# Kernel optimization log

Hardware: AMD Instinct MI355X
Metric: run time of the kernel (lower is better)

Reference implementation:

```python
import jax, jax.numpy as jnp
import numpy as np

B, S, D, H = 4, 1024, 512, 8
NEG = -1e9


def setup_inputs() -> dict:
    key = jax.random.key(0)
    ks = jax.random.split(key, 16)
    s = 0.02
    inp = {
        "query": jax.random.normal(ks[0], (B, S, D), dtype=jnp.float32),
        "key": jax.random.normal(ks[1], (B, S, D), dtype=jnp.float32),
        "value": jax.random.normal(ks[2], (B, S, D), dtype=jnp.float32),
        "mask": jax.random.randint(ks[3], (B, 1, S), 0, 2, dtype=jnp.int32),
        "mask_p": jax.random.randint(ks[4], (B, 1, S), 0, 2, dtype=jnp.int32),
        # multi-head projections: d_model -> d_model*h
        "Wq": jax.random.normal(ks[5], (D, H * D), dtype=jnp.float32) * s,
        "bq": jnp.zeros((H * D,), dtype=jnp.float32),
        "Wk": jax.random.normal(ks[6], (D, H * D), dtype=jnp.float32) * s,
        "bk": jnp.zeros((H * D,), dtype=jnp.float32),
        "Wv": jax.random.normal(ks[7], (D, H * D), dtype=jnp.float32) * s,
        "bv": jnp.zeros((H * D,), dtype=jnp.float32),
        # single-head p-branch projections: d_model -> d_model
        "Wpq": jax.random.normal(ks[8], (D, D), dtype=jnp.float32) * s,
        "bpq": jnp.zeros((D,), dtype=jnp.float32),
        "Wpk": jax.random.normal(ks[9], (D, D), dtype=jnp.float32) * s,
        "bpk": jnp.zeros((D,), dtype=jnp.float32),
        "Wpv": jax.random.normal(ks[10], (D, D), dtype=jnp.float32) * s,
        "bpv": jnp.zeros((D,), dtype=jnp.float32),
        # output projection
        "Wo": jax.random.normal(ks[11], (D, D), dtype=jnp.float32) * s,
        "bo": jnp.zeros((D,), dtype=jnp.float32),
    }
    return inp


def _attn(q, k, v, mask4):
    # q,k,v: [B,h,S,d]; mask4: [B,1,1,S] or None. Dropout omitted (eval mode).
    d = q.shape[-1]
    scores = jnp.einsum('bhqd,bhkd->bhqk', q, k) / jnp.sqrt(jnp.asarray(d, q.dtype))
    if mask4 is not None:
        scores = jnp.where(mask4 == 0, jnp.asarray(NEG, scores.dtype), scores)
    p = jax.nn.softmax(scores, axis=-1)
    return jnp.einsum('bhqk,bhkd->bhqd', p, v)


def reference(query, key, value, mask, mask_p,
              Wq, bq, Wk, bk, Wv, bv,
              Wpq, bpq, Wpk, bpk, Wpv, bpv, Wo, bo):
    nb, sl, d = query.shape
    def proj(x, W, b, heads):
        return (x @ W + b).reshape(nb, sl, heads, d).transpose(0, 2, 1, 3)

    m4 = mask[:, None, :, :]    # [B,1,1,S]
    mp4 = mask_p[:, None, :, :]

    qx = proj(query, Wq, bq, H)
    kx = proj(key, Wk, bk, H)
    vx = proj(value, Wv, bv, H)
    x = _attn(qx, kx, vx, m4)            # [B,H,S,D]

    qp = proj(query, Wpq, bpq, 1)
    kp = proj(key, Wpk, bpk, 1)
    vp = proj(value, Wpv, bpv, 1)
    x_p = _attn(qp, kp, vp, mp4)         # [B,1,S,D]

    # squared distance per head, softmax over heads at each (b, s)
    dis = jnp.sum((x - x_p) ** 2, axis=3)          # [B,H,S]
    w = jax.nn.softmax(1.0 / (dis + 1e-9), axis=1)  # [B,H,S]
    output = jnp.einsum('bhs,bhsd->bsd', w, x)      # [B,S,D]

    mixed = output * 0.8 + x_p[:, 0] * 0.2
    return mixed @ Wo + bo
```

## Files before the change

### kernel.cpp

```cpp
#include <hip/hip_runtime.h>
#include <cstdint>

#define S_LEN   1024
#define D_DIM   512
#define H_HEADS 8
#define B_BATCH 4
#define NEGV    -1000000000.0f

typedef __bf16 bf16;
typedef __bf16 bf16x8 __attribute__((ext_vector_type(8)));
typedef __bf16 bf16x4 __attribute__((ext_vector_type(4)));
typedef float  f32x4  __attribute__((ext_vector_type(4)));

#define GLL16(gp, lp) __builtin_amdgcn_global_load_lds( \
    (const __attribute__((address_space(1))) void*)(gp), \
    (__attribute__((address_space(3))) void*)(lp), 16, 0, 0)

template<int MODE>
__global__ __launch_bounds__(256) void gemm_bt(
    const bf16* __restrict__ A, const bf16* __restrict__ B,
    void* __restrict__ Cout, const float* __restrict__ bias,
    const float* __restrict__ bias2, const int* __restrict__ mask,
    int N, int K, long zsA, long zsB, long zsC, float scale, int Hh)
{
  const int z = blockIdx.z;
  A += (long)z * zsA;
  B += (long)z * zsB;

  const int bm0 = blockIdx.x * 128;
  const int bn0 = blockIdx.y * 128;

  __shared__ __attribute__((aligned(16))) bf16 As[128 * 32];
  __shared__ __attribute__((aligned(16))) bf16 Bs[128 * 32];

  const int tid  = threadIdx.x;
  const int wid  = tid >> 6;
  const int lane = tid & 63;
  const int wm = (wid >> 1) * 64;
  const int wn = (wid & 1) * 64;

  const int srow = tid >> 2;
  const int scol = (tid & 3) * 8;
  const bf16* gA0 = A + (long)(bm0 + srow) * K + scol;
  const bf16* gA1 = A + (long)(bm0 + 64 + srow) * K + scol;
  const bf16* gB0 = B + (long)(bn0 + srow) * K + scol;
  const bf16* gB1 = B + (long)(bn0 + 64 + srow) * K + scol;
  bf16* lA0 = As + tid * 8;
  bf16* lA1 = As + 2048 + tid * 8;
  bf16* lB0 = Bs + tid * 8;
  bf16* lB1 = Bs + 2048 + tid * 8;

  const int lrow = lane & 15;
  const int lk   = (lane >> 4) * 8;
  const bf16* fA = As + (wm + lrow) * 32 + lk;
  const bf16* fB = Bs + (wn + lrow) * 32 + lk;

  f32x4 acc[4][4] = {};

  for (int k0 = 0; k0 < K; k0 += 32) {
    GLL16(gA0 + k0, lA0);
    GLL16(gA1 + k0, lA1);
    GLL16(gB0 + k0, lB0);
    GLL16(gB1 + k0, lB1);
    __syncthreads();
    bf16x8 af[4], bfr[4];
#pragma unroll
    for (int i = 0; i < 4; ++i) af[i]  = *(const bf16x8*)(fA + i * 16 * 32);
#pragma unroll
    for (int i = 0; i < 4; ++i) bfr[i] = *(const bf16x8*)(fB + i * 16 * 32);
#pragma unroll
    for (int mi = 0; mi < 4; ++mi)
#pragma unroll
      for (int ni = 0; ni < 4; ++ni)
        acc[mi][ni] = __builtin_amdgcn_mfma_f32_16x16x32_bf16(
            af[mi], bfr[ni], acc[mi][ni], 0, 0, 0);
    __syncthreads();
  }

  const int r0 = (lane >> 4) << 2;
  const int cn = lane & 15;

#pragma unroll
  for (int mi = 0; mi < 4; ++mi) {
#pragma unroll
    for (int ni = 0; ni < 4; ++ni) {
      const int n = bn0 + wn + ni * 16 + cn;
      float bv = 0.f;
      if constexpr (MODE != 4) {
        const float* bp = (z == 1 && bias2) ? bias2 : bias;
        if (bp) bv = bp[n];
      }
      int mk = 1;
      if constexpr (MODE == 4) mk = mask[(z / Hh) * S_LEN + n];
#pragma unroll
      for (int r = 0; r < 4; ++r) {
        const int m = bm0 + wm + mi * 16 + r0 + r;
        float v = acc[mi][ni][r];
        if constexpr (MODE == 0) {
          ((bf16*)Cout)[(long)z * zsC + (long)m * N + n] = (bf16)(v + bv);
        } else if constexpr (MODE == 1) {
          long o = (long)z * zsC +
                   (((long)(m >> 10) * Hh + (n >> 9)) * S_LEN + (m & (S_LEN - 1))) * D_DIM
                   + (n & (D_DIM - 1));
          ((bf16*)Cout)[o] = (bf16)(v + bv);
        } else if constexpr (MODE == 2) {
          long o = (long)z * zsC +
                   (((long)(m >> 10) * Hh + (n >> 9)) * D_DIM + (n & (D_DIM - 1))) * S_LEN
                   + (m & (S_LEN - 1));
          ((bf16*)Cout)[o] = (bf16)(v + bv);
        } else if constexpr (MODE == 3) {
          ((float*)Cout)[(long)z * zsC + (long)m * N + n] = v + bv;
        } else {
          float sv = (mk == 0) ? NEGV : v * scale;
          ((bf16*)Cout)[(long)z * zsC + (long)m * N + n] = (bf16)sv;
        }
      }
    }
  }
}

__global__ __launch_bounds__(256) void softmax_rows(bf16* __restrict__ buf)
{
  const long row = blockIdx.x;
  bf16* p = buf + row * S_LEN;
  const int tid = threadIdx.x;
  const int wid = tid >> 6, lane = tid & 63;
  bf16x4 raw = *(const bf16x4*)(p + tid * 4);
  float v[4];
#pragma unroll
  for (int j = 0; j < 4; ++j) v[j] = (float)raw[j];
  float mx = fmaxf(fmaxf(v[0], v[1]), fmaxf(v[2], v[3]));
  for (int m = 32; m; m >>= 1) mx = fmaxf(mx, __shfl_xor(mx, m, 64));
  __shared__ float red[4];
  if (lane == 0) red[wid] = mx;
  __syncthreads();
  mx = fmaxf(fmaxf(red[0], red[1]), fmaxf(red[2], red[3]));
  float e[4]; float s = 0.f;
#pragma unroll
  for (int j = 0; j < 4; ++j) { e[j] = __expf(v[j] - mx); s += e[j]; }
  for (int m = 32; m; m >>= 1) s += __shfl_xor(s, m, 64);
  __syncthreads();
  if (lane == 0) red[wid] = s;
  __syncthreads();
  s = red[0] + red[1] + red[2] + red[3];
  const float inv = 1.f / s;
  bf16x4 o;
#pragma unroll
  for (int j = 0; j < 4; ++j) o[j] = (bf16)(e[j] * inv);
  *(bf16x4*)(p + tid * 4) = o;
}

__global__ __launch_bounds__(256) void combine_kernel(
    const float* __restrict__ X, const float* __restrict__ XP,
    bf16* __restrict__ MIX)
{
  const int m = blockIdx.x;
  const int b = m >> 10;
  const int s = m & (S_LEN - 1);
  const int tid = threadIdx.x;
  const int wid = tid >> 6, lane = tid & 63;
  const float2 xp = *(const float2*)(XP + (long)m * D_DIM + tid * 2);
  float xv0[H_HEADS], xv1[H_HEADS], part[H_HEADS];
#pragma unroll
  for (int h = 0; h < H_HEADS; ++h) {
    const float* xrow = X + ((long)(b * H_HEADS + h) * S_LEN + s) * D_DIM;
    float2 t = *(const float2*)(xrow + tid * 2);
    xv0[h] = t.x; xv1[h] = t.y;
    float d0 = t.x - xp.x, d1 = t.y - xp.y;
    part[h] = d0 * d0 + d1 * d1;
  }
  __shared__ float red[4][H_HEADS];
#pragma unroll
  for (int h = 0; h < H_HEADS; ++h) {
    float v = part[h];
    for (int mm = 32; mm; mm >>= 1) v += __shfl_xor(v, mm, 64);
    if (lane == 0) red[wid][h] = v;
  }
  __syncthreads();
  float w[H_HEADS]; float mx = -1e30f;
#pragma unroll
  for (int h = 0; h < H_HEADS; ++h) {
    float dis = red[0][h] + red[1][h] + red[2][h] + red[3][h];
    w[h] = 1.f / (dis + 1e-9f);
    mx = fmaxf(mx, w[h]);
  }
  float ssum = 0.f;
#pragma unroll
  for (int h = 0; h < H_HEADS; ++h) { w[h] = __expf(w[h] - mx); ssum += w[h]; }
  const float inv = 1.f / ssum;
  float m0 = 0.f, m1 = 0.f;
#pragma unroll
  for (int h = 0; h < H_HEADS; ++h) { m0 += w[h] * xv0[h]; m1 += w[h] * xv1[h]; }
  m0 = 0.8f * m0 * inv + 0.2f * xp.x;
  m1 = 0.8f * m1 * inv + 0.2f * xp.y;
  const bf16 h0 = (bf16)m0, h1 = (bf16)m1;
  const bf16 l0 = (bf16)(m0 - (float)h0), l1 = (bf16)(m1 - (float)h1);
  bf16* orow = MIX + (long)m * 1536;
  orow[tid * 2]        = h0; orow[tid * 2 + 1]        = h1;
  orow[512 + tid * 2]  = l0; orow[512 + tid * 2 + 1]  = l1;
  orow[1024 + tid * 2] = h0; orow[1024 + tid * 2 + 1] = h1;
}

__global__ __launch_bounds__(256) void cvt3_kernel(
    const float* __restrict__ s0, const float* __restrict__ s1, const float* __restrict__ s2,
    bf16* __restrict__ d0, bf16* __restrict__ d1, bf16* __restrict__ d2)
{
  const float* s = blockIdx.z == 0 ? s0 : (blockIdx.z == 1 ? s1 : s2);
  bf16* d       = blockIdx.z == 0 ? d0 : (blockIdx.z == 1 ? d1 : d2);
  const long i = ((long)blockIdx.x * 256 + threadIdx.x) * 8;
  float4 a = *(const float4*)(s + i);
  float4 b = *(const float4*)(s + i + 4);
  bf16x8 o;
  o[0]=(bf16)a.x; o[1]=(bf16)a.y; o[2]=(bf16)a.z; o[3]=(bf16)a.w;
  o[4]=(bf16)b.x; o[5]=(bf16)b.y; o[6]=(bf16)b.z; o[7]=(bf16)b.w;
  *(bf16x8*)(d + i) = o;
}

template<int TRIPLE>
__global__ __launch_bounds__(256) void transpose_cvt3(
    const float* __restrict__ s0, const float* __restrict__ s1, const float* __restrict__ s2,
    bf16* __restrict__ d0, bf16* __restrict__ d1, bf16* __restrict__ d2,
    int R, int C)
{
  const float* src = blockIdx.z == 0 ? s0 : (blockIdx.z == 1 ? s1 : s2);
  bf16* dst       = blockIdx.z == 0 ? d0 : (blockIdx.z == 1 ? d1 : d2);
  __shared__ float t[32][33];
  const int tc = threadIdx.x & 31;
  const int tr = threadIdx.x >> 5;
  const int c0 = blockIdx.x * 32, r0 = blockIdx.y * 32;
#pragma unroll
  for (int i = 0; i < 4; ++i)
    t[tr + 8 * i][tc] = src[(long)(r0 + tr + 8 * i) * C + c0 + tc];
  __syncthreads();
  const int RD = TRIPLE ? 3 * R : R;
#pragma unroll
  for (int i = 0; i < 4; ++i) {
    float v = t[tc][tr + 8 * i];
    long o = (long)(c0 + tr + 8 * i) * RD + r0 + tc;
    const bf16 hi = (bf16)v;
    dst[o] = hi;
    if (TRIPLE) {
      dst[o + R] = hi;
      dst[o + 2 * R] = (bf16)(v - (float)hi);
    }
  }
}

extern "C" void kernel_launch(void* const* d_in, const int* in_sizes, int n_in,
                              void* d_out, int out_size, void* d_ws, size_t ws_size,
                              hipStream_t stream) {
  const float* query  = (const float*)d_in[0];
  const float* key    = (const float*)d_in[1];
  const float* value  = (const float*)d_in[2];
  const int*   mask   = (const int*)d_in[3];
  const int*   mask_p = (const int*)d_in[4];
  const float* Wq  = (const float*)d_in[5];  const float* bq  = (const float*)d_in[6];
  const float* Wk  = (const float*)d_in[7];  const float* bk  = (const float*)d_in[8];
  const float* Wv  = (const float*)d_in[9];  const float* bv  = (const float*)d_in[10];
  const float* Wpq = (const float*)d_in[11]; const float* bpq = (const float*)d_in[12];
  const float* Wpk = (const float*)d_in[13]; const float* bpk = (const float*)d_in[14];
  const float* Wpv = (const float*)d_in[15]; const float* bpv = (const float*)d_in[16];
  const float* Wo  = (const float*)d_in[17]; const float* bo  = (const float*)d_in[18];

  char* ws = (char*)d_ws;
  size_t off = 0;
  auto alloc = [&](size_t bytes) -> void* {
    void* p = ws + off;
    off += (bytes + 255) & ~(size_t)255;
    return p;
  };
  const long BS  = (long)B_BATCH * S_LEN;
  const long ZSD = (long)S_LEN * D_DIM;
  const long ZSS = (long)S_LEN * S_LEN;
  const long SD  = BS * D_DIM;

  bf16* WQT  = (bf16*)alloc(SD * 2);
  bf16* WKT  = (bf16*)alloc(SD * 2);
  bf16* WVT  = (bf16*)alloc(SD * 2);
  bf16* WPQT = (bf16*)alloc((long)D_DIM * D_DIM * 2);
  bf16* WPKT = (bf16*)alloc((long)D_DIM * D_DIM * 2);
  bf16* WPVT = (bf16*)alloc((long)D_DIM * D_DIM * 2);
  bf16* WOT3 = (bf16*)alloc((long)D_DIM * 3 * D_DIM * 2);
  bf16* XQ16 = (bf16*)alloc(SD * 2);
  bf16* XK16 = (bf16*)alloc(SD * 2);
  bf16* XV16 = (bf16*)alloc(SD * 2);
  bf16* MIX  = XQ16;
  bf16* Q16  = (bf16*)alloc((long)H_HEADS * SD * 2);
  bf16* K16  = (bf16*)alloc((long)H_HEADS * SD * 2);
  float* X   = (float*)Q16;
  bf16* VT16 = (bf16*)alloc((long)H_HEADS * SD * 2);
  bf16* QP16 = (bf16*)alloc(SD * 2);
  bf16* KP16 = (bf16*)alloc(SD * 2);
  float* XP  = (float*)QP16;
  bf16* VPT16= (bf16*)alloc(SD * 2);
  bf16* SC   = (bf16*)alloc((long)B_BATCH * H_HEADS * ZSS * 2);
  bf16* SCP  = (bf16*)alloc((long)B_BATCH * ZSS * 2);
  (void)in_sizes; (void)n_in; (void)out_size; (void)SCP;

  if (off > ws_size) return;

  const dim3 blk(256);
  const float scale = 0.044194173824159216f;

  cvt3_kernel<<<dim3(1024, 1, 3), blk, 0, stream>>>(query, key, value, XQ16, XK16, XV16);
  transpose_cvt3<0><<<dim3(128, 16, 3), blk, 0, stream>>>(Wq, Wk, Wv, WQT, WKT, WVT, 512, 4096);
  transpose_cvt3<0><<<dim3(16, 16, 3), blk, 0, stream>>>(Wpq, Wpk, Wpv, WPQT, WPKT, WPVT, 512, 512);
  transpose_cvt3<1><<<dim3(16, 16, 1), blk, 0, stream>>>(Wo, Wo, Wo, WOT3, WOT3, WOT3, 512, 512);

  gemm_bt<1><<<dim3(32, 32, 2), blk, 0, stream>>>(XQ16, WQT, Q16, bq, bk, nullptr,
      4096, 512, SD, SD, (long)H_HEADS * SD, 1.f, H_HEADS);
  gemm_bt<2><<<dim3(32, 32, 1), blk, 0, stream>>>(XV16, WVT, VT16, bv, nullptr, nullptr,
      4096, 512, 0, 0, 0, 1.f, H_HEADS);
  gemm_bt<0><<<dim3(32, 4, 2), blk, 0, stream>>>(XQ16, WPQT, QP16, bpq, bpk, nullptr,
      512, 512, SD, (long)D_DIM * D_DIM, SD, 1.f, 1);
  gemm_bt<2><<<dim3(32, 4, 1), blk, 0, stream>>>(XV16, WPVT, VPT16, bpv, nullptr, nullptr,
      512, 512, 0, 0, 0, 1.f, 1);

  gemm_bt<4><<<dim3(8, 8, 32), blk, 0, stream>>>(Q16, K16, SC, nullptr, nullptr, mask,
      1024, 512, ZSD, ZSD, ZSS, scale, H_HEADS);
  gemm_bt<4><<<dim3(8, 8, 4), blk, 0, stream>>>(QP16, KP16, SCP, nullptr, nullptr, mask_p,
      1024, 512, ZSD, ZSD, ZSS, scale, 1);

  softmax_rows<<<dim3(32768 + 4096), blk, 0, stream>>>(SC);

  gemm_bt<3><<<dim3(8, 4, 32), blk, 0, stream>>>(SC, VT16, X, nullptr, nullptr, nullptr,
      512, 1024, ZSS, ZSD, ZSD, 1.f, 1);
  gemm_bt<3><<<dim3(8, 4, 4), blk, 0, stream>>>(SCP, VPT16, XP, nullptr, nullptr, nullptr,
      512, 1024, ZSS, ZSD, ZSD, 1.f, 1);

  combine_kernel<<<dim3(4096), blk, 0, stream>>>(X, XP, MIX);

  gemm_bt<3><<<dim3(32, 4, 1), blk, 0, stream>>>(MIX, WOT3, d_out, bo, nullptr, nullptr,
      512, 1536, 0, 0, 0, 1.f, 1);
}
```

Baseline: 524.1 us.

## Add 256x256-tile GEMM with 4-stage LDS pipeline and XCD-aware block remap

```diff
diff --git a/kernel.cpp b/kernel.cpp
--- a/kernel.cpp
+++ b/kernel.cpp
@@ -16,89 +16,130 @@
     (const __attribute__((address_space(1))) void*)(gp), \
     (__attribute__((address_space(3))) void*)(lp), 16, 0, 0)
 
+#define VMW(N) asm volatile("s_waitcnt vmcnt(" #N ")" ::: "memory")
+#define BARM() do { asm volatile("" ::: "memory"); \
+                    __builtin_amdgcn_s_barrier();  \
+                    asm volatile("" ::: "memory"); } while (0)
+
 template<int MODE>
-__global__ __launch_bounds__(256) void gemm_bt(
+__global__ __launch_bounds__(512, 2) void gemm256_bt(
     const bf16* __restrict__ A, const bf16* __restrict__ B,
     void* __restrict__ Cout, const float* __restrict__ bias,
     const float* __restrict__ bias2, const int* __restrict__ mask,
     int N, int K, long zsA, long zsB, long zsC, float scale, int Hh)
 {
-  const int z = blockIdx.z;
+  const int gx = gridDim.x, gy = gridDim.y;
+  const int nwg = gx * gy * gridDim.z;
+  int bid = blockIdx.x + gx * (blockIdx.y + gy * blockIdx.z);
+  {
+    const int q = nwg >> 3, r = nwg & 7;
+    const int xcd = bid & 7, idx = bid >> 3;
+    bid = (xcd < r ? xcd * (q + 1) : r * (q + 1) + (xcd - r) * q) + idx;
+  }
+  const int bx = bid % gx;
+  const int by = (bid / gx) % gy;
+  const int z  = bid / (gx * gy);
+
   A += (long)z * zsA;
   B += (long)z * zsB;
-
-  const int bm0 = blockIdx.x * 128;
-  const int bn0 = blockIdx.y * 128;
-
-  __shared__ __attribute__((aligned(16))) bf16 As[128 * 32];
-  __shared__ __attribute__((aligned(16))) bf16 Bs[128 * 32];
+  const int bm0 = bx * 256;
+  const int bn0 = by * 256;
+
+  __shared__ __attribute__((aligned(16))) bf16 LDS[4 * 16384];
 
   const int tid  = threadIdx.x;
   const int wid  = tid >> 6;
   const int lane = tid & 63;
-  const int wm = (wid >> 1) * 64;
-  const int wn = (wid & 1) * 64;
-
-  const int srow = tid >> 2;
-  const int scol = (tid & 3) * 8;
-  const bf16* gA0 = A + (long)(bm0 + srow) * K + scol;
-  const bf16* gA1 = A + (long)(bm0 + 64 + srow) * K + scol;
-  const bf16* gB0 = B + (long)(bn0 + srow) * K + scol;
-  const bf16* gB1 = B + (long)(bn0 + 64 + srow) * K + scol;
-  bf16* lA0 = As + tid * 8;
-  bf16* lA1 = As + 2048 + tid * 8;
-  bf16* lB0 = Bs + tid * 8;
-  bf16* lB1 = Bs + 2048 + tid * 8;
-
-  const int lrow = lane & 15;
-  const int lk   = (lane >> 4) * 8;
-  const bf16* fA = As + (wm + lrow) * 32 + lk;
-  const bf16* fB = Bs + (wn + lrow) * 32 + lk;
-
-  f32x4 acc[4][4] = {};
-
-  for (int k0 = 0; k0 < K; k0 += 32) {
-    GLL16(gA0 + k0, lA0);
-    GLL16(gA1 + k0, lA1);
-    GLL16(gB0 + k0, lB0);
-    GLL16(gB1 + k0, lB1);
-    __syncthreads();
-    bf16x8 af[4], bfr[4];
-#pragma unroll
-    for (int i = 0; i < 4; ++i) af[i]  = *(const bf16x8*)(fA + i * 16 * 32);
-#pragma unroll
-    for (int i = 0; i < 4; ++i) bfr[i] = *(const bf16x8*)(fB + i * 16 * 32);
+  const int wr = wid >> 2;
+  const int wc = wid & 3;
+
+  const long arow = (long)(bm0 + wid * 16 + (lane & 15)) * K + ((lane >> 4) * 8);
+  const long brow = (long)(bn0 + wid * 16 + (lane & 15)) * K + ((lane >> 4) * 8);
+  const long rstep = 128L * (long)K;
+
+  auto stageA = [&](int tt) {
+    bf16* d = LDS + (tt & 3) * 16384 + wid * 512;
+    const bf16* g = A + arow + (long)tt * 32;
+    GLL16(g, d);
+    GLL16(g + rstep, d + 4096);
+  };
+  auto stageB = [&](int tt) {
+    bf16* d = LDS + (tt & 3) * 16384 + 8192 + wid * 512;
+    const bf16* g = B + brow + (long)tt * 32;
+    GLL16(g, d);
+    GLL16(g + rstep, d + 4096);
+  };
+
+  f32x4 acc[8][4] = {};
+  const int NT = K >> 5;
+
+  stageA(0); stageB(0);
+  stageA(1); stageB(1);
+  stageA(2); stageB(2);
+  VMW(8);
+  BARM();
+
+  for (int t = 0; t < NT; ++t) {
+    const bf16* bufp = LDS + (t & 3) * 16384;
+    const bf16* ap = bufp + wr * 4096 + lane * 8;
+    const bf16* bp = bufp + 8192 + wc * 2048 + lane * 8;
+
+    if (t + 3 < NT) stageA(t + 3);
+    bf16x8 a0[4], bb[4];
+#pragma unroll
+    for (int i = 0; i < 4; ++i) a0[i] = *(const bf16x8*)(ap + i * 512);
+#pragma unroll
+    for (int i = 0; i < 4; ++i) bb[i] = *(const bf16x8*)(bp + i * 512);
+    BARM();
+    __builtin_amdgcn_s_setprio(1);
 #pragma unroll
     for (int mi = 0; mi < 4; ++mi)
 #pragma unroll
       for (int ni = 0; ni < 4; ++ni)
         acc[mi][ni] = __builtin_amdgcn_mfma_f32_16x16x32_bf16(
-            af[mi], bfr[ni], acc[mi][ni], 0, 0, 0);
-    __syncthreads();
+            a0[mi], bb[ni], acc[mi][ni], 0, 0, 0);
+    __builtin_amdgcn_s_setprio(0);
+    BARM();
+
+    if (t + 3 < NT) stageB(t + 3);
+    bf16x8 a1[4];
+#pragma unroll
+    for (int i = 0; i < 4; ++i) a1[i] = *(const bf16x8*)(ap + (4 + i) * 512);
+    BARM();
+    __builtin_amdgcn_s_setprio(1);
+#pragma unroll
+    for (int mi = 0; mi < 4; ++mi)
+#pragma unroll
+      for (int ni = 0; ni < 4; ++ni)
+        acc[4 + mi][ni] = __builtin_amdgcn_mfma_f32_16x16x32_bf16(
+            a1[mi], bb[ni], acc[4 + mi][ni], 0, 0, 0);
+    __builtin_amdgcn_s_setprio(0);
+    if (t <= NT - 4)      VMW(8);
+    else if (t == NT - 3) VMW(4);
+    else if (t == NT - 2) VMW(0);
+    BARM();
   }
 
   const int r0 = (lane >> 4) << 2;
   const int cn = lane & 15;
 
 #pragma unroll
-  for (int mi = 0; mi < 4; ++mi) {
+  for (int mi = 0; mi < 8; ++mi) {
 #pragma unroll
     for (int ni = 0; ni < 4; ++ni) {
-      const int n = bn0 + wn + ni * 16 + cn;
+      const int n = bn0 + wc * 64 + ni * 16 + cn;
       float bv = 0.f;
       if constexpr (MODE != 4) {
-        const float* bp = (z == 1 && bias2) ? bias2 : bias;
-        if (bp) bv = bp[n];
+        const float* bp2 = (z == 1 && bias2) ? bias2 : bias;
+        if (bp2) bv = bp2[n];
       }
       int mk = 1;
       if constexpr (MODE == 4) mk = mask[(z / Hh) * S_LEN + n];
 #pragma unroll
       for (int r = 0; r < 4; ++r) {
-        const int m = bm0 + wm + mi * 16 + r0 + r;
+        const int m = bm0 + wr * 128 + mi * 16 + r0 + r;
         float v = acc[mi][ni][r];
-        if constexpr (MODE == 0) {
-          ((bf16*)Cout)[(long)z * zsC + (long)m * N + n] = (bf16)(v + bv);
-        } else if constexpr (MODE == 1) {
+        if constexpr (MODE == 1) {
           long o = (long)z * zsC +
                    (((long)(m >> 10) * Hh + (n >> 9)) * S_LEN + (m & (S_LEN - 1))) * D_DIM
                    + (n & (D_DIM - 1));
@@ -111,6 +152,104 @@
         } else if constexpr (MODE == 3) {
           ((float*)Cout)[(long)z * zsC + (long)m * N + n] = v + bv;
         } else {
+          float sv = (mk == 0) ? NEGV : v * scale;
+          ((bf16*)Cout)[(long)z * zsC + (long)m * N + n] = (bf16)sv;
+        }
+      }
+    }
+  }
+}
+
+template<int MODE>
+__global__ __launch_bounds__(256) void gemm_bt(
+    const bf16* __restrict__ A, const bf16* __restrict__ B,
+    void* __restrict__ Cout, const float* __restrict__ bias,
+    const float* __restrict__ bias2, const int* __restrict__ mask,
+    int N, int K, long zsA, long zsB, long zsC, float scale, int Hh)
+{
+  const int z = blockIdx.z;
+  A += (long)z * zsA;
+  B += (long)z * zsB;
+
+  const int bm0 = blockIdx.x * 128;
+  const int bn0 = blockIdx.y * 128;
+
+  __shared__ __attribute__((aligned(16))) bf16 As[128 * 32];
+  __shared__ __attribute__((aligned(16))) bf16 Bs[128 * 32];
+
+  const int tid  = threadIdx.x;
+  const int wid  = tid >> 6;
+  const int lane = tid & 63;
+  const int wm = (wid >> 1) * 64;
+  const int wn = (wid & 1) * 64;
+
+  const int srow = tid >> 2;
+  const int scol = (tid & 3) * 8;
+  const bf16* gA0 = A + (long)(bm0 + srow) * K + scol;
+  const bf16* gA1 = A + (long)(bm0 + 64 + srow) * K + scol;
+  const bf16* gB0 = B + (long)(bn0 + srow) * K + scol;
+  const bf16* gB1 = B + (long)(bn0 + 64 + srow) * K + scol;
+  bf16* lA0 = As + tid * 8;
+  bf16* lA1 = As + 2048 + tid * 8;
+  bf16* lB0 = Bs + tid * 8;
+  bf16* lB1 = Bs + 2048 + tid * 8;
+
+  const int lrow = lane & 15;
+  const int lk   = (lane >> 4) * 8;
+  const bf16* fA = As + (wm + lrow) * 32 + lk;
+  const bf16* fB = Bs + (wn + lrow) * 32 + lk;
+
+  f32x4 acc[4][4] = {};
+
+  for (int k0 = 0; k0 < K; k0 += 32) {
+    GLL16(gA0 + k0, lA0);
+    GLL16(gA1 + k0, lA1);
+    GLL16(gB0 + k0, lB0);
+    GLL16(gB1 + k0, lB1);
+    __syncthreads();
+    bf16x8 af[4], bfr[4];
+#pragma unroll
+    for (int i = 0; i < 4; ++i) af[i]  = *(const bf16x8*)(fA + i * 16 * 32);
+#pragma unroll
+    for (int i = 0; i < 4; ++i) bfr[i] = *(const bf16x8*)(fB + i * 16 * 32);
+#pragma unroll
+    for (int mi = 0; mi < 4; ++mi)
+#pragma unroll
+      for (int ni = 0; ni < 4; ++ni)
+        acc[mi][ni] = __builtin_amdgcn_mfma_f32_16x16x32_bf16(
+            af[mi], bfr[ni], acc[mi][ni], 0, 0, 0);
+    __syncthreads();
+  }
+
+  const int r0 = (lane >> 4) << 2;
+  const int cn = lane & 15;
+
+#pragma unroll
+  for (int mi = 0; mi < 4; ++mi) {
+#pragma unroll
+    for (int ni = 0; ni < 4; ++ni) {
+      const int n = bn0 + wn + ni * 16 + cn;
+      float bv = 0.f;
+      if constexpr (MODE != 4) {
+        const float* bp = (z == 1 && bias2) ? bias2 : bias;
+        if (bp) bv = bp[n];
+      }
+      int mk = 1;
+      if constexpr (MODE == 4) mk = mask[(z / Hh) * S_LEN + n];
+#pragma unroll
+      for (int r = 0; r < 4; ++r) {
+        const int m = bm0 + wm + mi * 16 + r0 + r;
+        float v = acc[mi][ni][r];
+        if constexpr (MODE == 0) {
+          ((bf16*)Cout)[(long)z * zsC + (long)m * N + n] = (bf16)(v + bv);
+        } else if constexpr (MODE == 2) {
+          long o = (long)z * zsC +
+                   (((long)(m >> 10) * Hh + (n >> 9)) * D_DIM + (n & (D_DIM - 1))) * S_LEN
+                   + (m & (S_LEN - 1));
+          ((bf16*)Cout)[o] = (bf16)(v + bv);
+        } else if constexpr (MODE == 3) {
+          ((float*)Cout)[(long)z * zsC + (long)m * N + n] = v + bv;
+        } else if constexpr (MODE == 4) {
           float sv = (mk == 0) ? NEGV : v * scale;
           ((bf16*)Cout)[(long)z * zsC + (long)m * N + n] = (bf16)sv;
         }
@@ -300,6 +439,7 @@
   if (off > ws_size) return;
 
   const dim3 blk(256);
+  const dim3 blk512(512);
   const float scale = 0.044194173824159216f;
 
   cvt3_kernel<<<dim3(1024, 1, 3), blk, 0, stream>>>(query, key, value, XQ16, XK16, XV16);
@@ -307,23 +447,23 @@
   transpose_cvt3<0><<<dim3(16, 16, 3), blk, 0, stream>>>(Wpq, Wpk, Wpv, WPQT, WPKT, WPVT, 512, 512);
   transpose_cvt3<1><<<dim3(16, 16, 1), blk, 0, stream>>>(Wo, Wo, Wo, WOT3, WOT3, WOT3, 512, 512);
 
-  gemm_bt<1><<<dim3(32, 32, 2), blk, 0, stream>>>(XQ16, WQT, Q16, bq, bk, nullptr,
+  gemm256_bt<1><<<dim3(16, 16, 2), blk512, 0, stream>>>(XQ16, WQT, Q16, bq, bk, nullptr,
       4096, 512, SD, SD, (long)H_HEADS * SD, 1.f, H_HEADS);
-  gemm_bt<2><<<dim3(32, 32, 1), blk, 0, stream>>>(XV16, WVT, VT16, bv, nullptr, nullptr,
+  gemm256_bt<2><<<dim3(16, 16, 1), blk512, 0, stream>>>(XV16, WVT, VT16, bv, nullptr, nullptr,
       4096, 512, 0, 0, 0, 1.f, H_HEADS);
   gemm_bt<0><<<dim3(32, 4, 2), blk, 0, stream>>>(XQ16, WPQT, QP16, bpq, bpk, nullptr,
       512, 512, SD, (long)D_DIM * D_DIM, SD, 1.f, 1);
   gemm_bt<2><<<dim3(32, 4, 1), blk, 0, stream>>>(XV16, WPVT, VPT16, bpv, nullptr, nullptr,
       512, 512, 0, 0, 0, 1.f, 1);
 
-  gemm_bt<4><<<dim3(8, 8, 32), blk, 0, stream>>>(Q16, K16, SC, nullptr, nullptr, mask,
+  gemm256_bt<4><<<dim3(4, 4, 32), blk512, 0, stream>>>(Q16, K16, SC, nullptr, nullptr, mask,
       1024, 512, ZSD, ZSD, ZSS, scale, H_HEADS);
   gemm_bt<4><<<dim3(8, 8, 4), blk, 0, stream>>>(QP16, KP16, SCP, nullptr, nullptr, mask_p,
       1024, 512, ZSD, ZSD, ZSS, scale, 1);
 
   softmax_rows<<<dim3(32768 + 4096), blk, 0, stream>>>(SC);
 
-  gemm_bt<3><<<dim3(8, 4, 32), blk, 0, stream>>>(SC, VT16, X, nullptr, nullptr, nullptr,
+  gemm256_bt<3><<<dim3(4, 2, 32), blk512, 0, stream>>>(SC, VT16, X, nullptr, nullptr, nullptr,
       512, 1024, ZSS, ZSD, ZSD, 1.f, 1);
   gemm_bt<3><<<dim3(8, 4, 4), blk, 0, stream>>>(SCP, VPT16, XP, nullptr, nullptr, nullptr,
       512, 1024, ZSS, ZSD, ZSD, 1.f, 1);
```

Result: faster. 477.7 us (-8.9%).
